# Kernel optimization log

Hardware: AMD Instinct MI355X
Metric: run time of the kernel (lower is better)

Reference implementation:

```python
import jax, jax.numpy as jnp
import numpy as np

N, E = 100000, 1600000
IN, H, OUT = 64, 64, 32
BN_EPS = 1e-5


def setup_inputs() -> dict:
    key = jax.random.key(0)
    ks = jax.random.split(key, 13)

    def w(k, shape, fan_in):
        return jax.random.uniform(k, shape, jnp.float32, -1.0, 1.0) / np.sqrt(fan_in)

    return {
        "x": jax.random.normal(ks[0], (N, IN), jnp.float32),
        "edge_index": jax.random.randint(ks[1], (2, E), 0, N, jnp.int32),
        "W1": w(ks[2], (IN, H), IN),
        "b1": jnp.zeros((H,), jnp.float32),
        "gamma": jnp.ones((H,), jnp.float32),
        "beta": jnp.zeros((H,), jnp.float32),
        "W2": w(ks[3], (H, H), H),
        "b2": jnp.zeros((H,), jnp.float32),
        "lin2_w": w(ks[4], (H, OUT), H),
        "lin2_b": w(ks[5], (OUT,), H),
        "lin3_w": w(ks[6], (OUT, H), OUT),
        "lin3_b": w(ks[7], (H,), OUT),
    }


def gcn_conv(x, src, dst, W, b):
    # PyG GCNConv: h = D^{-1/2} (A + I) D^{-1/2} (x W) + b
    n = x.shape[0]
    h = x @ W  # [N, H]
    loop = jnp.arange(n, dtype=src.dtype)
    s = jnp.concatenate([src, loop])  # add self-loops
    d = jnp.concatenate([dst, loop])
    deg = jax.ops.segment_sum(jnp.ones_like(s, x.dtype), d, num_segments=n)
    dinv = jnp.where(deg > 0, jax.lax.rsqrt(deg), 0.0)
    norm = dinv[s] * dinv[d]  # [E+N]
    msg = h[s] * norm[:, None]  # gather + scale
    out = jax.ops.segment_sum(msg, d, num_segments=n)  # scatter-add
    return out + b


def reference(x, edge_index, W1, b1, gamma, beta, W2, b2, lin2_w, lin2_b, lin3_w, lin3_b):
    src, dst = edge_index[0], edge_index[1]
    h = gcn_conv(x, src, dst, W1, b1)
    # BatchNorm1d in eval mode with default running stats (mean=0, var=1)
    h = gamma * (h * jax.lax.rsqrt(jnp.float32(1.0 + BN_EPS))) + beta
    h = jax.nn.relu(h)  # dropout is identity in eval
    h = gcn_conv(h, src, dst, W2, b2)
    logits = h @ lin2_w + lin2_b  # [N, OUT]
    p = jax.nn.softmax(logits, axis=-1)
    ent = -jnp.sum(p * jnp.log(p + 1e-9), axis=-1)  # [N]
    wts = 1.0 / (ent + 1e-10)
    wts = (wts - wts.min()) / (wts.max() - wts.min())
    wts = jax.nn.softmax(wts, axis=0)  # [N]
    graph = jnp.sum(logits * wts[:, None], axis=0, keepdims=True)  # [1, OUT]
    return graph @ lin3_w + lin3_b  # [1, H]
```

## Files before the change

kernel.cpp:

```cpp
#include <hip/hip_runtime.h>
#include <hip/hip_bf16.h>
#include <hip/hip_fp8.h>
#include <math.h>


#define F 64
#define OUTF 32
#define PB 128
#define LEDGE 5632
#define WG 512
#define BN_INV 0.9999950000374997f
#define ESC_X 32.0f
#define IESC_X 0.03125f
#define ESC_Z 64.0f
#define IESC_Z 0.015625f

typedef short bf16x8 __attribute__((ext_vector_type(8)));
typedef float f32x4 __attribute__((ext_vector_type(4)));

__device__ __forceinline__ unsigned fenc(float f) {
    unsigned u = __float_as_uint(f);
    return (u & 0x80000000u) ? ~u : (u | 0x80000000u);
}
__device__ __forceinline__ float fdec(unsigned e) {
    return (e & 0x80000000u) ? __uint_as_float(e & 0x7fffffffu) : __uint_as_float(~e);
}
__device__ __forceinline__ unsigned short f2bf(float f) {
    unsigned u = __float_as_uint(f);
    return (unsigned short)((u + 0x7fffu + ((u >> 16) & 1u)) >> 16);
}
__device__ __forceinline__ float bf2f(unsigned short h) {
    return __uint_as_float((unsigned)h << 16);
}

#if __has_builtin(__builtin_amdgcn_cvt_f32_fp8) && __has_builtin(__builtin_amdgcn_cvt_pk_fp8_f32)
__device__ __forceinline__ float4 fp8x4(unsigned v) {
    return make_float4(__builtin_amdgcn_cvt_f32_fp8((int)v, 0),
                       __builtin_amdgcn_cvt_f32_fp8((int)v, 1),
                       __builtin_amdgcn_cvt_f32_fp8((int)v, 2),
                       __builtin_amdgcn_cvt_f32_fp8((int)v, 3));
}
__device__ __forceinline__ unsigned fp8pk4(float a, float b, float c, float d) {
    int r = __builtin_amdgcn_cvt_pk_fp8_f32(a, b, 0, false);
    r = __builtin_amdgcn_cvt_pk_fp8_f32(c, d, r, true);
    return (unsigned)r;
}
__device__ __forceinline__ unsigned char fp8enc1(float a) {
    return (unsigned char)(__builtin_amdgcn_cvt_pk_fp8_f32(a, a, 0, false) & 0xff);
}
#else
__device__ __forceinline__ float fp8d1(unsigned char b) {
    __hip_fp8_e4m3 v; v.__x = (__hip_fp8_storage_t)b; return (float)v;
}
__device__ __forceinline__ float4 fp8x4(unsigned v) {
    return make_float4(fp8d1(v & 255u), fp8d1((v >> 8) & 255u), fp8d1((v >> 16) & 255u), fp8d1((v >> 24) & 255u));
}
__device__ __forceinline__ unsigned char fp8enc1(float a) {
    return (unsigned char)__hip_fp8_e4m3(a).__x;
}
__device__ __forceinline__ unsigned fp8pk4(float a, float b, float c, float d) {
    return (unsigned)fp8enc1(a) | ((unsigned)fp8enc1(b) << 8) | ((unsigned)fp8enc1(c) << 16) | ((unsigned)fp8enc1(d) << 24);
}
#endif


__global__ __launch_bounds__(256) void k_hist(const int* __restrict__ dst, int* __restrict__ hist,
                                              int E, int NBK,
                                              const float* __restrict__ W1, const float* __restrict__ b1,
                                              const float* __restrict__ gamma, const float* __restrict__ beta,
                                              const float* __restrict__ W2, const float* __restrict__ b2,
                                              const float* __restrict__ l2w, const float* __restrict__ l2b,
                                              unsigned short* __restrict__ w1f, unsigned short* __restrict__ w2f,
                                              float* __restrict__ bias1f, float* __restrict__ b2l2,
                                              float* __restrict__ red) {
    __shared__ int lh[512];
    int t = threadIdx.x, blk = blockIdx.x;
    if (blk >= PB) {
        int tt = (blk - PB) * 256 + t;
        int k = tt >> 5, cc = tt & 31;
        float o = 0.0f;
        for (int j = 0; j < F; j++) o += W2[k * F + j] * l2w[j * OUTF + cc];
        {
            int t2 = cc >> 4, s = k >> 5, kb = (k >> 3) & 3, jj = k & 7;
            int ln = kb * 16 + (cc & 15);
            w2f[(size_t)((t2 * 2 + s) * 64 + ln) * 8 + jj] = f2bf(o);
        }
        for (int e = tt; e < F * F; e += 2048) {
            int kk = e >> 6, c = e & 63;
            float wv = W1[kk * F + c] * gamma[c] * BN_INV;
            int t1i = c >> 4, s = kk >> 5, kb = (kk >> 3) & 3, jj = kk & 7;
            int ln = kb * 16 + (c & 15);
            w1f[(size_t)((t1i * 2 + s) * 64 + ln) * 8 + jj] = f2bf(wv);
        }
        if (tt < F) bias1f[tt] = fmaf(b1[tt], gamma[tt] * BN_INV, beta[tt]);
        if (tt < OUTF) {
            float b = l2b[tt];
            for (int j = 0; j < F; j++) b += b2[j] * l2w[j * OUTF + tt];
            b2l2[tt] = b;
        }
        if (tt == 33) ((unsigned*)red)[33] = 0xFFFFFFFFu;
        if (tt == 34) ((unsigned*)red)[34] = 0u;
        return;
    }
    for (int b = t; b < NBK; b += 256) lh[b] = 0;
    __syncthreads();
    int chunk = (E + PB - 1) / PB;
    int beg = blk * chunk, end = min(beg + chunk, E);
    for (int e = beg + t; e < end; e += 256) atomicAdd(&lh[dst[e] >> 8], 1);
    __syncthreads();
    for (int b = t; b < NBK; b += 256) hist[blk * NBK + b] = lh[b];
}

__global__ __launch_bounds__(PB) void k_hscan1(int* __restrict__ hist, int* __restrict__ btot, int NBK) {
    __shared__ int s[PB];
    int b = blockIdx.x, t = threadIdx.x;
    int v = hist[t * NBK + b];
    s[t] = v;
    __syncthreads();
    for (int off = 1; off < PB; off <<= 1) {
        int u = (t >= off) ? s[t - off] : 0;
        __syncthreads();
        s[t] += u;
        __syncthreads();
    }
    hist[t * NBK + b] = s[t] - v;
    if (t == PB - 1) btot[b] = s[t];
}

__global__ void k_hscan2(const int* __restrict__ btot, int* __restrict__ bbase, int NBK) {
    __shared__ int s[512];
    int t = threadIdx.x;
    int v = (t < NBK) ? btot[t] : 0;
    s[t] = v;
    __syncthreads();
    for (int off = 1; off < 512; off <<= 1) {
        int u = (t >= off) ? s[t - off] : 0;
        __syncthreads();
        s[t] += u;
        __syncthreads();
    }
    if (t < NBK) {
        bbase[t] = s[t] - v;
        if (t == NBK - 1) bbase[NBK] = s[t];
    }
}

__global__ __launch_bounds__(256) void k_place(const int* __restrict__ src, const int* __restrict__ dst,
                                               const int* __restrict__ hist, const int* __restrict__ bbase,
                                               unsigned* __restrict__ bucketArr, int E, int NBK) {
    __shared__ int cur[512];
    int t = threadIdx.x, blk = blockIdx.x;
    for (int b = t; b < NBK; b += 256) cur[b] = hist[blk * NBK + b] + bbase[b];
    __syncthreads();
    int chunk = (E + PB - 1) / PB;
    int beg = blk * chunk, end = min(beg + chunk, E);
    for (int e = beg + t; e < end; e += 256) {
        int d = dst[e], sidx = src[e];
        int p = atomicAdd(&cur[d >> 8], 1);
        bucketArr[p] = ((unsigned)sidx << 8) | (unsigned)(d & 255);
    }
}

__global__ __launch_bounds__(256) void k_binsort(const unsigned* __restrict__ bucketArr,
                                                 const int* __restrict__ bbase,
                                                 int* __restrict__ eidx, int4* __restrict__ meta,
                                                 const float4* __restrict__ x4, unsigned* __restrict__ xq, int N) {
    __shared__ unsigned ledge[LEDGE];
    __shared__ int lcnt[256], lofs[256], lcur[256], lscan[256];
    __shared__ float ldinv[256];
    int b = blockIdx.x, t = threadIdx.x;
    int gb = bbase[b];
    int count = min(bbase[b + 1] - gb, LEDGE);
    for (int j = t; j < count; j += 256) ledge[j] = bucketArr[gb + j];
    lcnt[t] = 0;
    __syncthreads();
    for (int j = t; j < count; j += 256) atomicAdd(&lcnt[ledge[j] & 255u], 1);
    __syncthreads();
    int deg = lcnt[t];
    lscan[t] = deg;
    __syncthreads();
    for (int off = 1; off < 256; off <<= 1) {
        int u = (t >= off) ? lscan[t - off] : 0;
        __syncthreads();
        lscan[t] += u;
        __syncthreads();
    }
    lofs[t] = lscan[t] - deg;
    lcur[t] = 0;
    int node = (b << 8) + t;
    float di = rsqrtf((float)deg + 1.0f);
    ldinv[t] = di;
    if (node < N) meta[node] = make_int4(gb + lofs[t], deg, __float_as_int(di), 0);
    __syncthreads();
    for (int j = t; j < count; j += 256) {
        unsigned v = ledge[j];
        int loc = (int)(v & 255u);
        int p = atomicAdd(&lcur[loc], 1);
        eidx[gb + lofs[loc] + p] = (int)(v >> 8);
    }
    for (int idx = t; idx < 256 * 16; idx += 256) {
        int nd = (b << 8) + (idx >> 4);
        if (nd < N) {
            float d2 = ldinv[idx >> 4] * ESC_X;
            float4 v = x4[(size_t)nd * 16 + (idx & 15)];
            xq[(size_t)nd * 16 + (idx & 15)] = fp8pk4(v.x * d2, v.y * d2, v.z * d2, v.w * d2);
        }
    }
}

__global__ __launch_bounds__(256, 4) void k_conv1agg(const uint2* __restrict__ xq2,
                                                     const int4* __restrict__ meta,
                                                     const int* __restrict__ eidx,
                                                     unsigned short* __restrict__ t1, int N, int Em1) {
    int tid = threadIdx.x, wave = tid >> 6, lane = tid & 63;
    int g = lane >> 3, gl = lane & 7, gbase = lane & 56;
    int i = (blockIdx.x * 4 + wave) * 8 + g;
    int iclamp = min(i, N - 1);
    int4 m = meta[iclamp];
    int beg = m.x;
    int dcnt = (i < N) ? m.y : 0;
    float dis = __int_as_float(m.z) * IESC_X;
    int ss0 = eidx[min(beg + gl, Em1)];
    int ss1 = eidx[min(beg + 8 + gl, Em1)];
    int ss2 = eidx[min(beg + 16 + gl, Em1)];
    int ss3 = eidx[min(beg + 24 + gl, Em1)];
    uint2 selfv = xq2[(size_t)iclamp * 8 + gl];
    uint2 vbuf[32];
#pragma unroll
    for (int k = 0; k < 32; k++) {
        int sreg = (k < 8) ? ss0 : (k < 16) ? ss1 : (k < 24) ? ss2 : ss3;
        int sv = __shfl(sreg, gbase + (k & 7), 64);
        sv = (k < dcnt) ? sv : iclamp;
        vbuf[k] = xq2[(size_t)sv * 8 + gl];
    }
    __builtin_amdgcn_sched_barrier(0);
    float4 aA0 = fp8x4(selfv.x), aB0 = fp8x4(selfv.y);
    float4 aA1 = make_float4(0.f, 0.f, 0.f, 0.f), aB1 = aA1;
#pragma unroll
    for (int k = 0; k < 32; k++) {
        if (k < dcnt) {
            float4 vA = fp8x4(vbuf[k].x), vB = fp8x4(vbuf[k].y);
            if (k & 1) {
                aA1.x += vA.x; aA1.y += vA.y; aA1.z += vA.z; aA1.w += vA.w;
                aB1.x += vB.x; aB1.y += vB.y; aB1.z += vB.z; aB1.w += vB.w;
            } else {
                aA0.x += vA.x; aA0.y += vA.y; aA0.z += vA.z; aA0.w += vA.w;
                aB0.x += vB.x; aB0.y += vB.y; aB0.z += vB.z; aB0.w += vB.w;
            }
        }
    }
    for (int base = 32; base < dcnt; base += 8) {
        int j = base + gl;
        int ss = eidx[min(beg + j, Em1)];
        int cnt = min(dcnt - base, 8);
#pragma unroll
        for (int k = 0; k < 8; k++) {
            if (k < cnt) {
                int sv = __shfl(ss, gbase + k, 64);
                uint2 v = xq2[(size_t)sv * 8 + gl];
                float4 vA = fp8x4(v.x), vB = fp8x4(v.y);
                aA0.x += vA.x; aA0.y += vA.y; aA0.z += vA.z; aA0.w += vA.w;
                aB0.x += vB.x; aB0.y += vB.y; aB0.z += vB.z; aB0.w += vB.w;
            }
        }
    }
    if (i < N) {
        float4 oA, oB;
        oA.x = (aA0.x + aA1.x) * dis; oA.y = (aA0.y + aA1.y) * dis;
        oA.z = (aA0.z + aA1.z) * dis; oA.w = (aA0.w + aA1.w) * dis;
        oB.x = (aB0.x + aB1.x) * dis; oB.y = (aB0.y + aB1.y) * dis;
        oB.z = (aB0.z + aB1.z) * dis; oB.w = (aB0.w + aB1.w) * dis;
        uint4 ob;
        ob.x = (unsigned)f2bf(oA.x) | ((unsigned)f2bf(oA.y) << 16);
        ob.y = (unsigned)f2bf(oA.z) | ((unsigned)f2bf(oA.w) << 16);
        ob.z = (unsigned)f2bf(oB.x) | ((unsigned)f2bf(oB.y) << 16);
        ob.w = (unsigned)f2bf(oB.z) | ((unsigned)f2bf(oB.w) << 16);
        *(uint4*)(t1 + (size_t)i * F + gl * 8) = ob;
    }
}

__global__ __launch_bounds__(256) void k_zm(const unsigned short* __restrict__ t1bf,
                                            const int4* __restrict__ meta,
                                            const unsigned short* __restrict__ w1f,
                                            const unsigned short* __restrict__ w2f,
                                            const float* __restrict__ bias1f,
                                            unsigned char* __restrict__ z2q, int N) {
    __shared__ __align__(16) unsigned short hlds[4][16][72];
    __shared__ float ldin[4][16];
    int tid = threadIdx.x, wave = tid >> 6, lane = tid & 63;
    int cl = lane & 15, kb = lane >> 4;
    int ntiles = (N + 15) >> 4;
    int tile = blockIdx.x * 4 + wave;
    if (tile >= ntiles) return;
    int row0 = tile << 4;

    int ra = min(row0 + cl, N - 1);
    const bf16x8* arow = (const bf16x8*)(t1bf + (size_t)ra * F);
    bf16x8 a0 = arow[kb];
    bf16x8 a1 = arow[4 + kb];
    if (lane < 16) ldin[wave][lane] = __int_as_float(meta[min(row0 + lane, N - 1)].z);

    const bf16x8* w1v = (const bf16x8*)w1f;
    const bf16x8* w2v = (const bf16x8*)w2f;
    bf16x8 w1frag[8];
#pragma unroll
    for (int q = 0; q < 8; q++) w1frag[q] = w1v[q * 64 + lane];
    bf16x8 w2frag[4];
#pragma unroll
    for (int q = 0; q < 4; q++) w2frag[q] = w2v[q * 64 + lane];
    float bias_t[4];
#pragma unroll
    for (int t = 0; t < 4; t++) bias_t[t] = bias1f[t * 16 + cl];

    f32x4 acc[4] = {};
#pragma unroll
    for (int t = 0; t < 4; t++) {
        acc[t] = __builtin_amdgcn_mfma_f32_16x16x32_bf16(a0, w1frag[t * 2 + 0], acc[t], 0, 0, 0);
        acc[t] = __builtin_amdgcn_mfma_f32_16x16x32_bf16(a1, w1frag[t * 2 + 1], acc[t], 0, 0, 0);
    }
    float di[4];
#pragma unroll
    for (int j = 0; j < 4; j++) di[j] = ldin[wave][kb * 4 + j];
#pragma unroll
    for (int t = 0; t < 4; t++)
#pragma unroll
        for (int j = 0; j < 4; j++) {
            float h = fmaxf(acc[t][j] + bias_t[t], 0.0f) * di[j];
            hlds[wave][kb * 4 + j][t * 16 + cl] = f2bf(h);
        }
    bf16x8 h0 = *(const bf16x8*)&hlds[wave][cl][kb * 8];
    bf16x8 h1 = *(const bf16x8*)&hlds[wave][cl][32 + kb * 8];
    f32x4 accz[2] = {};
#pragma unroll
    for (int t2 = 0; t2 < 2; t2++) {
        accz[t2] = __builtin_amdgcn_mfma_f32_16x16x32_bf16(h0, w2frag[t2 * 2 + 0], accz[t2], 0, 0, 0);
        accz[t2] = __builtin_amdgcn_mfma_f32_16x16x32_bf16(h1, w2frag[t2 * 2 + 1], accz[t2], 0, 0, 0);
    }
#pragma unroll
    for (int t2 = 0; t2 < 2; t2++)
#pragma unroll
        for (int j = 0; j < 4; j++) {
            int r = row0 + kb * 4 + j;
            if (r < N) z2q[(size_t)r * OUTF + t2 * 16 + cl] = fp8enc1(accz[t2][j] * ESC_Z);
        }
}

__global__ __launch_bounds__(256, 4) void k_conv2agg(const uint2* __restrict__ z2q2,
                                                     const int4* __restrict__ meta,
                                                     const int* __restrict__ eidx, const float* __restrict__ b2l2,
                                                     unsigned short* __restrict__ logits_bf, float* __restrict__ wraw,
                                                     unsigned* __restrict__ redmm, int N, int Em1) {
    __shared__ float smn[4], smx[4];
    int tid = threadIdx.x, wave = tid >> 6, lane = tid & 63;
    int g = lane >> 2, gl = lane & 3, gbase = lane & 60;
    float4 bvA = ((const float4*)b2l2)[gl * 2];
    float4 bvB = ((const float4*)b2l2)[gl * 2 + 1];
    int i = (blockIdx.x * 4 + wave) * 16 + g;
    int iclamp = min(i, N - 1);
    int4 m = meta[iclamp];
    int beg = m.x;
    int dcnt = (i < N) ? m.y : 0;
    float dis = __int_as_float(m.z) * IESC_Z;
    int ss0 = eidx[min(beg + gl, Em1)];
    int ss1 = eidx[min(beg + 4 + gl, Em1)];
    int ss2 = eidx[min(beg + 8 + gl, Em1)];
    int ss3 = eidx[min(beg + 12 + gl, Em1)];
    int ss4 = eidx[min(beg + 16 + gl, Em1)];
    int ss5 = eidx[min(beg + 20 + gl, Em1)];
    uint2 selfv = z2q2[(size_t)iclamp * 4 + gl];
    uint2 vbuf[24];
#pragma unroll
    for (int k = 0; k < 24; k++) {
        int sreg = (k < 4) ? ss0 : (k < 8) ? ss1 : (k < 12) ? ss2 : (k < 16) ? ss3 : (k < 20) ? ss4 : ss5;
        int sv = __shfl(sreg, gbase + (k & 3), 64);
        sv = (k < dcnt) ? sv : iclamp;
        vbuf[k] = z2q2[(size_t)sv * 4 + gl];
    }
    __builtin_amdgcn_sched_barrier(0);
    float4 aA0 = fp8x4(selfv.x), aB0 = fp8x4(selfv.y);
    if (i >= N) { aA0 = make_float4(0.f, 0.f, 0.f, 0.f); aB0 = aA0; }
    float4 aA1 = make_float4(0.f, 0.f, 0.f, 0.f), aB1 = aA1;
#pragma unroll
    for (int k = 0; k < 24; k++) {
        if (k < dcnt) {
            float4 vA = fp8x4(vbuf[k].x), vB = fp8x4(vbuf[k].y);
            if (k & 1) {
                aA1.x += vA.x; aA1.y += vA.y; aA1.z += vA.z; aA1.w += vA.w;
                aB1.x += vB.x; aB1.y += vB.y; aB1.z += vB.z; aB1.w += vB.w;
            } else {
                aA0.x += vA.x; aA0.y += vA.y; aA0.z += vA.z; aA0.w += vA.w;
                aB0.x += vB.x; aB0.y += vB.y; aB0.z += vB.z; aB0.w += vB.w;
            }
        }
    }
    for (int base = 24; base < dcnt; base += 4) {
        int j = base + gl;
        int ss = eidx[min(beg + j, Em1)];
        int cnt = min(dcnt - base, 4);
#pragma unroll
        for (int k = 0; k < 4; k++) {
            if (k < cnt) {
                int sv = __shfl(ss, gbase + k, 64);
                uint2 v = z2q2[(size_t)sv * 4 + gl];
                float4 vA = fp8x4(v.x), vB = fp8x4(v.y);
                aA0.x += vA.x; aA0.y += vA.y; aA0.z += vA.z; aA0.w += vA.w;
                aB0.x += vB.x; aB0.y += vB.y; aB0.z += vB.z; aB0.w += vB.w;
            }
        }
    }
    float4 lgA, lgB;
    lgA.x = fmaf(aA0.x + aA1.x, dis, bvA.x);
    lgA.y = fmaf(aA0.y + aA1.y, dis, bvA.y);
    lgA.z = fmaf(aA0.z + aA1.z, dis, bvA.z);
    lgA.w = fmaf(aA0.w + aA1.w, dis, bvA.w);
    lgB.x = fmaf(aB0.x + aB1.x, dis, bvB.x);
    lgB.y = fmaf(aB0.y + aB1.y, dis, bvB.y);
    lgB.z = fmaf(aB0.z + aB1.z, dis, bvB.z);
    lgB.w = fmaf(aB0.w + aB1.w, dis, bvB.w);
    if (i < N) {
        uint4 ob;
        ob.x = (unsigned)f2bf(lgA.x) | ((unsigned)f2bf(lgA.y) << 16);
        ob.y = (unsigned)f2bf(lgA.z) | ((unsigned)f2bf(lgA.w) << 16);
        ob.z = (unsigned)f2bf(lgB.x) | ((unsigned)f2bf(lgB.y) << 16);
        ob.w = (unsigned)f2bf(lgB.z) | ((unsigned)f2bf(lgB.w) << 16);
        *(uint4*)(logits_bf + (size_t)i * OUTF + gl * 8) = ob;
    }
    float m8 = fmaxf(fmaxf(fmaxf(lgA.x, lgA.y), fmaxf(lgA.z, lgA.w)),
                     fmaxf(fmaxf(lgB.x, lgB.y), fmaxf(lgB.z, lgB.w)));
    for (int off = 2; off > 0; off >>= 1) m8 = fmaxf(m8, __shfl_xor(m8, off, 4));
    float p0 = expf(lgA.x - m8), p1 = expf(lgA.y - m8), p2 = expf(lgA.z - m8), p3 = expf(lgA.w - m8);
    float p4 = expf(lgB.x - m8), p5 = expf(lgB.y - m8), p6 = expf(lgB.z - m8), p7 = expf(lgB.w - m8);
    float s8 = p0 + p1 + p2 + p3 + p4 + p5 + p6 + p7;
    for (int off = 2; off > 0; off >>= 1) s8 += __shfl_xor(s8, off, 4);
    float inv = 1.0f / s8;
    float t0 = p0 * inv, t1v = p1 * inv, t2v = p2 * inv, t3 = p3 * inv;
    float t4 = p4 * inv, t5 = p5 * inv, t6 = p6 * inv, t7 = p7 * inv;
    float e8 = t0 * logf(t0 + 1e-9f) + t1v * logf(t1v + 1e-9f) + t2v * logf(t2v + 1e-9f) + t3 * logf(t3 + 1e-9f) +
               t4 * logf(t4 + 1e-9f) + t5 * logf(t5 + 1e-9f) + t6 * logf(t6 + 1e-9f) + t7 * logf(t7 + 1e-9f);
    for (int off = 2; off > 0; off >>= 1) e8 += __shfl_xor(e8, off, 4);
    float w = 1.0f / (-e8 + 1e-10f);
    float mn = INFINITY, mx = -INFINITY;
    if (i < N) {
        if (gl == 0) wraw[i] = w;
        mn = w;
        mx = w;
    }
    for (int off = 32; off > 0; off >>= 1) {
        mn = fminf(mn, __shfl_xor(mn, off, 64));
        mx = fmaxf(mx, __shfl_xor(mx, off, 64));
    }
    if (lane == 0) { smn[wave] = mn; smx[wave] = mx; }
    __syncthreads();
    if (tid == 0) {
        float a = fminf(fminf(smn[0], smn[1]), fminf(smn[2], smn[3]));
        float b = fmaxf(fmaxf(smx[0], smx[1]), fmaxf(smx[2], smx[3]));
        atomicMin(&redmm[33], fenc(a));
        atomicMax(&redmm[34], fenc(b));
    }
}

__global__ __launch_bounds__(256) void k_weight(const unsigned short* __restrict__ logits_bf,
                                                const float* __restrict__ wraw,
                                                const float* __restrict__ red,
                                                float* __restrict__ part, int N) {
    const unsigned* mm = (const unsigned*)red;
    float mn = fdec(mm[33]), mx = fdec(mm[34]);
    float inv = 1.0f / (mx - mn);
    int c = threadIdx.x & 31;
    int g = threadIdx.x >> 5;
    float acc = 0.0f, es = 0.0f;
    for (int r = blockIdx.x * 8 + g; r < N; r += gridDim.x * 8) {
        float e = expf((wraw[r] - mn) * inv);
        acc += e * bf2f(logits_bf[(size_t)r * OUTF + c]);
        if (c == 0) es += e;
    }
    __shared__ float sa[8][OUTF];
    __shared__ float se[8];
    sa[g][c] = acc;
    if (c == 0) se[g] = es;
    __syncthreads();
    if (g == 0) {
        float t = sa[0][c];
#pragma unroll
        for (int i = 1; i < 8; i++) t += sa[i][c];
        part[blockIdx.x * 36 + c] = t;
        if (c == 0) {
            float u = 0.0f;
#pragma unroll
            for (int i = 0; i < 8; i++) u += se[i];
            part[blockIdx.x * 36 + 32] = u;
        }
    }
}

__global__ __launch_bounds__(256) void k_final(const float* __restrict__ part,
                                               const float* __restrict__ w3, const float* __restrict__ b3,
                                               float* __restrict__ out) {
    __shared__ float sa[8][OUTF];
    __shared__ float se[8];
    __shared__ float facc[OUTF + 1];
    int tid = threadIdx.x;
    int g = tid >> 5, c = tid & 31;
    float acc = 0.0f, es = 0.0f;
    for (int p = g; p < WG; p += 8) {
        acc += part[p * 36 + c];
        if (c == 0) es += part[p * 36 + 32];
    }
    sa[g][c] = acc;
    if (c == 0) se[g] = es;
    __syncthreads();
    if (tid < OUTF) {
        float t = 0.0f;
#pragma unroll
        for (int i = 0; i < 8; i++) t += sa[i][tid];
        facc[tid] = t;
    }
    if (tid == 32) {
        float u = 0.0f;
#pragma unroll
        for (int i = 0; i < 8; i++) u += se[i];
        facc[OUTF] = u;
    }
    __syncthreads();
    if (tid < F) {
        float s = facc[OUTF];
        float o = b3[tid];
#pragma unroll
        for (int cc = 0; cc < OUTF; cc++) o += (facc[cc] / s) * w3[cc * F + tid];
        out[tid] = o;
    }
}

extern "C" void kernel_launch(void* const* d_in, const int* in_sizes, int n_in,
                              void* d_out, int out_size, void* d_ws, size_t ws_size,
                              hipStream_t stream) {
    const float* x     = (const float*)d_in[0];
    const int*   ei    = (const int*)d_in[1];
    const float* W1    = (const float*)d_in[2];
    const float* b1    = (const float*)d_in[3];
    const float* gamma = (const float*)d_in[4];
    const float* beta  = (const float*)d_in[5];
    const float* W2    = (const float*)d_in[6];
    const float* b2    = (const float*)d_in[7];
    const float* l2w   = (const float*)d_in[8];
    const float* l2b   = (const float*)d_in[9];
    const float* l3w   = (const float*)d_in[10];
    const float* l3b   = (const float*)d_in[11];

    int N = in_sizes[0] / F;
    int E = in_sizes[1] / 2;
    const int* src = ei;
    const int* dst = ei + E;
    int NBK = (N + 255) >> 8;

    char* p = (char*)d_ws;
    int* hist = (int*)p;                p += (size_t)PB * NBK * 4;
    int* btot = (int*)p;                p += 512 * 4;
    int* bbase = (int*)p;               p += 516 * 4;
    unsigned* bucketArr = (unsigned*)p; p += (size_t)E * 4;
    int4* meta = (int4*)p;              p += (size_t)N * 16;
    int* eidx = (int*)p;                p += (size_t)E * 4;
    float* red = (float*)p;             p += 64 * 4;
    float* part = (float*)p;            p += (size_t)WG * 36 * 4;
    unsigned short* w1f = (unsigned short*)p;  p += F * F * 2;
    unsigned short* w2f = (unsigned short*)p;  p += F * OUTF * 2;
    float* bias1f = (float*)p;          p += F * 4;
    float* b2l2 = (float*)p;            p += OUTF * 4 + 32;
    unsigned* xq = (unsigned*)p;        p += (size_t)N * F;
    unsigned short* t1bf = (unsigned short*)p; p += (size_t)N * F * 2;
    float* wraw = (float*)p;            p += (size_t)N * 4;
    unsigned char* z2q = (unsigned char*)xq;
    unsigned short* logits_bf = (unsigned short*)t1bf;

    k_hist<<<PB + 8, 256, 0, stream>>>(dst, hist, E, NBK, W1, b1, gamma, beta, W2, b2, l2w, l2b,
                                       w1f, w2f, bias1f, b2l2, red);
    k_hscan1<<<NBK, PB, 0, stream>>>(hist, btot, NBK);
    k_hscan2<<<1, 512, 0, stream>>>(btot, bbase, NBK);
    k_place<<<PB, 256, 0, stream>>>(src, dst, hist, bbase, bucketArr, E, NBK);
    k_binsort<<<NBK, 256, 0, stream>>>(bucketArr, bbase, eidx, meta, (const float4*)x, xq, N);

    k_conv1agg<<<(N + 31) / 32, 256, 0, stream>>>((const uint2*)xq, meta, eidx, t1bf, N, E - 1);
    int nt = (N + 15) >> 4;
    k_zm<<<(nt + 3) / 4, 256, 0, stream>>>(t1bf, meta, w1f, w2f, bias1f, z2q, N);
    k_conv2agg<<<(N + 63) / 64, 256, 0, stream>>>((const uint2*)z2q, meta, eidx, b2l2, logits_bf, wraw, (unsigned*)red, N, E - 1);

    k_weight<<<WG, 256, 0, stream>>>(logits_bf, wraw, red, part, N);
    k_final<<<1, 256, 0, stream>>>(part, l3w, l3b, (float*)d_out);
}
```

Measured before the change: 263.2 us.

## Process two node groups per wave in conv2 aggregation and drop atomic min/max

k_conv2agg now has each wave handle 32 nodes instead of 16. It issues both groups' neighbor gathers before consuming either, aiming for more memory-level parallelism per wave, and launch bounds drop to 2 blocks per SM to make room for the extra registers. The global atomic min/max on encoded floats is replaced by per-block partial min/max that k_weight reduces itself, which removes the reset in k_hist. expf/logf become the fast __expf/__logf intrinsics, trading some accuracy for cheaper transcendentals.

```diff
diff --git a/kernel.cpp b/kernel.cpp
--- a/kernel.cpp
+++ b/kernel.cpp
@@ -18,13 +18,6 @@
 typedef short bf16x8 __attribute__((ext_vector_type(8)));
 typedef float f32x4 __attribute__((ext_vector_type(4)));
 
-__device__ __forceinline__ unsigned fenc(float f) {
-    unsigned u = __float_as_uint(f);
-    return (u & 0x80000000u) ? ~u : (u | 0x80000000u);
-}
-__device__ __forceinline__ float fdec(unsigned e) {
-    return (e & 0x80000000u) ? __uint_as_float(e & 0x7fffffffu) : __uint_as_float(~e);
-}
 __device__ __forceinline__ unsigned short f2bf(float f) {
     unsigned u = __float_as_uint(f);
     return (unsigned short)((u + 0x7fffu + ((u >> 16) & 1u)) >> 16);
@@ -62,7 +55,6 @@
     return (unsigned)fp8enc1(a) | ((unsigned)fp8enc1(b) << 8) | ((unsigned)fp8enc1(c) << 16) | ((unsigned)fp8enc1(d) << 24);
 }
 #endif
-
 
 __global__ __launch_bounds__(256) void k_hist(const int* __restrict__ dst, int* __restrict__ hist,
                                               int E, int NBK,
@@ -71,8 +63,7 @@
                                               const float* __restrict__ W2, const float* __restrict__ b2,
                                               const float* __restrict__ l2w, const float* __restrict__ l2b,
                                               unsigned short* __restrict__ w1f, unsigned short* __restrict__ w2f,
-                                              float* __restrict__ bias1f, float* __restrict__ b2l2,
-                                              float* __restrict__ red) {
+                                              float* __restrict__ bias1f, float* __restrict__ b2l2) {
     __shared__ int lh[512];
     int t = threadIdx.x, blk = blockIdx.x;
     if (blk >= PB) {
@@ -98,8 +89,6 @@
             for (int j = 0; j < F; j++) b += b2[j] * l2w[j * OUTF + tt];
             b2l2[tt] = b;
         }
-        if (tt == 33) ((unsigned*)red)[33] = 0xFFFFFFFFu;
-        if (tt == 34) ((unsigned*)red)[34] = 0u;
         return;
     }
     for (int b = t; b < NBK; b += 256) lh[b] = 0;
@@ -345,38 +334,13 @@
         }
 }
 
-__global__ __launch_bounds__(256, 4) void k_conv2agg(const uint2* __restrict__ z2q2,
-                                                     const int4* __restrict__ meta,
-                                                     const int* __restrict__ eidx, const float* __restrict__ b2l2,
-                                                     unsigned short* __restrict__ logits_bf, float* __restrict__ wraw,
-                                                     unsigned* __restrict__ redmm, int N, int Em1) {
-    __shared__ float smn[4], smx[4];
-    int tid = threadIdx.x, wave = tid >> 6, lane = tid & 63;
-    int g = lane >> 2, gl = lane & 3, gbase = lane & 60;
-    float4 bvA = ((const float4*)b2l2)[gl * 2];
-    float4 bvB = ((const float4*)b2l2)[gl * 2 + 1];
-    int i = (blockIdx.x * 4 + wave) * 16 + g;
-    int iclamp = min(i, N - 1);
-    int4 m = meta[iclamp];
-    int beg = m.x;
-    int dcnt = (i < N) ? m.y : 0;
-    float dis = __int_as_float(m.z) * IESC_Z;
-    int ss0 = eidx[min(beg + gl, Em1)];
-    int ss1 = eidx[min(beg + 4 + gl, Em1)];
-    int ss2 = eidx[min(beg + 8 + gl, Em1)];
-    int ss3 = eidx[min(beg + 12 + gl, Em1)];
-    int ss4 = eidx[min(beg + 16 + gl, Em1)];
-    int ss5 = eidx[min(beg + 20 + gl, Em1)];
-    uint2 selfv = z2q2[(size_t)iclamp * 4 + gl];
-    uint2 vbuf[24];
-#pragma unroll
-    for (int k = 0; k < 24; k++) {
-        int sreg = (k < 4) ? ss0 : (k < 8) ? ss1 : (k < 12) ? ss2 : (k < 16) ? ss3 : (k < 20) ? ss4 : ss5;
-        int sv = __shfl(sreg, gbase + (k & 3), 64);
-        sv = (k < dcnt) ? sv : iclamp;
-        vbuf[k] = z2q2[(size_t)sv * 4 + gl];
-    }
-    __builtin_amdgcn_sched_barrier(0);
+__device__ __forceinline__ void conv2_consume(const uint2 (&vbuf)[24], uint2 selfv, int dcnt,
+                                              int i, int beg, float dis, int gl, int gbase,
+                                              const uint2* __restrict__ z2q2, const int* __restrict__ eidx,
+                                              int Em1, float4 bvA, float4 bvB,
+                                              unsigned short* __restrict__ logits_bf,
+                                              float* __restrict__ wraw,
+                                              float& mnW, float& mxW, int N) {
     float4 aA0 = fp8x4(selfv.x), aB0 = fp8x4(selfv.y);
     if (i >= N) { aA0 = make_float4(0.f, 0.f, 0.f, 0.f); aB0 = aA0; }
     float4 aA1 = make_float4(0.f, 0.f, 0.f, 0.f), aB1 = aA1;
@@ -428,49 +392,116 @@
     float m8 = fmaxf(fmaxf(fmaxf(lgA.x, lgA.y), fmaxf(lgA.z, lgA.w)),
                      fmaxf(fmaxf(lgB.x, lgB.y), fmaxf(lgB.z, lgB.w)));
     for (int off = 2; off > 0; off >>= 1) m8 = fmaxf(m8, __shfl_xor(m8, off, 4));
-    float p0 = expf(lgA.x - m8), p1 = expf(lgA.y - m8), p2 = expf(lgA.z - m8), p3 = expf(lgA.w - m8);
-    float p4 = expf(lgB.x - m8), p5 = expf(lgB.y - m8), p6 = expf(lgB.z - m8), p7 = expf(lgB.w - m8);
+    float p0 = __expf(lgA.x - m8), p1 = __expf(lgA.y - m8), p2 = __expf(lgA.z - m8), p3 = __expf(lgA.w - m8);
+    float p4 = __expf(lgB.x - m8), p5 = __expf(lgB.y - m8), p6 = __expf(lgB.z - m8), p7 = __expf(lgB.w - m8);
     float s8 = p0 + p1 + p2 + p3 + p4 + p5 + p6 + p7;
     for (int off = 2; off > 0; off >>= 1) s8 += __shfl_xor(s8, off, 4);
     float inv = 1.0f / s8;
     float t0 = p0 * inv, t1v = p1 * inv, t2v = p2 * inv, t3 = p3 * inv;
     float t4 = p4 * inv, t5 = p5 * inv, t6 = p6 * inv, t7 = p7 * inv;
-    float e8 = t0 * logf(t0 + 1e-9f) + t1v * logf(t1v + 1e-9f) + t2v * logf(t2v + 1e-9f) + t3 * logf(t3 + 1e-9f) +
-               t4 * logf(t4 + 1e-9f) + t5 * logf(t5 + 1e-9f) + t6 * logf(t6 + 1e-9f) + t7 * logf(t7 + 1e-9f);
+    float e8 = t0 * __logf(t0 + 1e-9f) + t1v * __logf(t1v + 1e-9f) + t2v * __logf(t2v + 1e-9f) + t3 * __logf(t3 + 1e-9f) +
+               t4 * __logf(t4 + 1e-9f) + t5 * __logf(t5 + 1e-9f) + t6 * __logf(t6 + 1e-9f) + t7 * __logf(t7 + 1e-9f);
     for (int off = 2; off > 0; off >>= 1) e8 += __shfl_xor(e8, off, 4);
     float w = 1.0f / (-e8 + 1e-10f);
-    float mn = INFINITY, mx = -INFINITY;
     if (i < N) {
         if (gl == 0) wraw[i] = w;
-        mn = w;
-        mx = w;
+        mnW = fminf(mnW, w);
+        mxW = fmaxf(mxW, w);
+    }
+}
+
+__global__ __launch_bounds__(256, 2) void k_conv2agg(const uint2* __restrict__ z2q2,
+                                                     const int4* __restrict__ meta,
+                                                     const int* __restrict__ eidx, const float* __restrict__ b2l2,
+                                                     unsigned short* __restrict__ logits_bf, float* __restrict__ wraw,
+                                                     float* __restrict__ mnmx, int N, int Em1) {
+    __shared__ float smn[4], smx[4];
+    int tid = threadIdx.x, wave = tid >> 6, lane = tid & 63;
+    int g = lane >> 2, gl = lane & 3, gbase = lane & 60;
+    float4 bvA = ((const float4*)b2l2)[gl * 2];
+    float4 bvB = ((const float4*)b2l2)[gl * 2 + 1];
+    int wgid = blockIdx.x * 4 + wave;
+    int i0 = wgid * 32 + g;
+    int i1 = wgid * 32 + 16 + g;
+    int i0c = min(i0, N - 1), i1c = min(i1, N - 1);
+    int4 m0 = meta[i0c], m1 = meta[i1c];
+    int beg0 = m0.x, beg1 = m1.x;
+    int d0 = (i0 < N) ? m0.y : 0;
+    int d1 = (i1 < N) ? m1.y : 0;
+    float dis0 = __int_as_float(m0.z) * IESC_Z;
+    float dis1 = __int_as_float(m1.z) * IESC_Z;
+    int sA0 = eidx[min(beg0 + gl, Em1)];
+    int sA1 = eidx[min(beg0 + 4 + gl, Em1)];
+    int sA2 = eidx[min(beg0 + 8 + gl, Em1)];
+    int sA3 = eidx[min(beg0 + 12 + gl, Em1)];
+    int sA4 = eidx[min(beg0 + 16 + gl, Em1)];
+    int sA5 = eidx[min(beg0 + 20 + gl, Em1)];
+    int sB0 = eidx[min(beg1 + gl, Em1)];
+    int sB1 = eidx[min(beg1 + 4 + gl, Em1)];
+    int sB2 = eidx[min(beg1 + 8 + gl, Em1)];
+    int sB3 = eidx[min(beg1 + 12 + gl, Em1)];
+    int sB4 = eidx[min(beg1 + 16 + gl, Em1)];
+    int sB5 = eidx[min(beg1 + 20 + gl, Em1)];
+    uint2 self0 = z2q2[(size_t)i0c * 4 + gl];
+    uint2 self1 = z2q2[(size_t)i1c * 4 + gl];
+    uint2 vb0[24], vb1[24];
+#pragma unroll
+    for (int k = 0; k < 24; k++) {
+        int sreg = (k < 4) ? sA0 : (k < 8) ? sA1 : (k < 12) ? sA2 : (k < 16) ? sA3 : (k < 20) ? sA4 : sA5;
+        int sv = __shfl(sreg, gbase + (k & 3), 64);
+        sv = (k < d0) ? sv : i0c;
+        vb0[k] = z2q2[(size_t)sv * 4 + gl];
+    }
+#pragma unroll
+    for (int k = 0; k < 24; k++) {
+        int sreg = (k < 4) ? sB0 : (k < 8) ? sB1 : (k < 12) ? sB2 : (k < 16) ? sB3 : (k < 20) ? sB4 : sB5;
+        int sv = __shfl(sreg, gbase + (k & 3), 64);
+        sv = (k < d1) ? sv : i1c;
+        vb1[k] = z2q2[(size_t)sv * 4 + gl];
+    }
+    __builtin_amdgcn_sched_barrier(0);
+    float mnW = INFINITY, mxW = -INFINITY;
+    conv2_consume(vb0, self0, d0, i0, beg0, dis0, gl, gbase, z2q2, eidx, Em1,
+                  bvA, bvB, logits_bf, wraw, mnW, mxW, N);
+    conv2_consume(vb1, self1, d1, i1, beg1, dis1, gl, gbase, z2q2, eidx, Em1,
+                  bvA, bvB, logits_bf, wraw, mnW, mxW, N);
+    for (int off = 32; off > 0; off >>= 1) {
+        mnW = fminf(mnW, __shfl_xor(mnW, off, 64));
+        mxW = fmaxf(mxW, __shfl_xor(mxW, off, 64));
+    }
+    if (lane == 0) { smn[wave] = mnW; smx[wave] = mxW; }
+    __syncthreads();
+    if (tid == 0) {
+        mnmx[blockIdx.x * 2]     = fminf(fminf(smn[0], smn[1]), fminf(smn[2], smn[3]));
+        mnmx[blockIdx.x * 2 + 1] = fmaxf(fmaxf(smx[0], smx[1]), fmaxf(smx[2], smx[3]));
+    }
+}
+
+__global__ __launch_bounds__(256) void k_weight(const unsigned short* __restrict__ logits_bf,
+                                                const float* __restrict__ wraw,
+                                                const float* __restrict__ mnmx, int nmm,
+                                                float* __restrict__ part, int N) {
+    __shared__ float rmn[4], rmx[4];
+    float mn = INFINITY, mx = -INFINITY;
+    for (int j = threadIdx.x; j < nmm; j += 256) {
+        mn = fminf(mn, mnmx[j * 2]);
+        mx = fmaxf(mx, mnmx[j * 2 + 1]);
     }
     for (int off = 32; off > 0; off >>= 1) {
         mn = fminf(mn, __shfl_xor(mn, off, 64));
         mx = fmaxf(mx, __shfl_xor(mx, off, 64));
     }
-    if (lane == 0) { smn[wave] = mn; smx[wave] = mx; }
-    __syncthreads();
-    if (tid == 0) {
-        float a = fminf(fminf(smn[0], smn[1]), fminf(smn[2], smn[3]));
-        float b = fmaxf(fmaxf(smx[0], smx[1]), fmaxf(smx[2], smx[3]));
-        atomicMin(&redmm[33], fenc(a));
-        atomicMax(&redmm[34], fenc(b));
-    }
-}
-
-__global__ __launch_bounds__(256) void k_weight(const unsigned short* __restrict__ logits_bf,
-                                                const float* __restrict__ wraw,
-                                                const float* __restrict__ red,
-                                                float* __restrict__ part, int N) {
-    const unsigned* mm = (const unsigned*)red;
-    float mn = fdec(mm[33]), mx = fdec(mm[34]);
+    int wv = threadIdx.x >> 6;
+    if ((threadIdx.x & 63) == 0) { rmn[wv] = mn; rmx[wv] = mx; }
+    __syncthreads();
+    mn = fminf(fminf(rmn[0], rmn[1]), fminf(rmn[2], rmn[3]));
+    mx = fmaxf(fmaxf(rmx[0], rmx[1]), fmaxf(rmx[2], rmx[3]));
     float inv = 1.0f / (mx - mn);
     int c = threadIdx.x & 31;
     int g = threadIdx.x >> 5;
     float acc = 0.0f, es = 0.0f;
     for (int r = blockIdx.x * 8 + g; r < N; r += gridDim.x * 8) {
-        float e = expf((wraw[r] - mn) * inv);
+        float e = __expf((wraw[r] - mn) * inv);
         acc += e * bf2f(logits_bf[(size_t)r * OUTF + c]);
         if (c == 0) es += e;
     }
@@ -560,7 +591,7 @@
     unsigned* bucketArr = (unsigned*)p; p += (size_t)E * 4;
     int4* meta = (int4*)p;              p += (size_t)N * 16;
     int* eidx = (int*)p;                p += (size_t)E * 4;
-    float* red = (float*)p;             p += 64 * 4;
+    float* mnmx = (float*)p;            p += 2048 * 4;
     float* part = (float*)p;            p += (size_t)WG * 36 * 4;
     unsigned short* w1f = (unsigned short*)p;  p += F * F * 2;
     unsigned short* w2f = (unsigned short*)p;  p += F * OUTF * 2;
@@ -573,7 +604,7 @@
     unsigned short* logits_bf = (unsigned short*)t1bf;
 
     k_hist<<<PB + 8, 256, 0, stream>>>(dst, hist, E, NBK, W1, b1, gamma, beta, W2, b2, l2w, l2b,
-                                       w1f, w2f, bias1f, b2l2, red);
+                                       w1f, w2f, bias1f, b2l2);
     k_hscan1<<<NBK, PB, 0, stream>>>(hist, btot, NBK);
     k_hscan2<<<1, 512, 0, stream>>>(btot, bbase, NBK);
     k_place<<<PB, 256, 0, stream>>>(src, dst, hist, bbase, bucketArr, E, NBK);
@@ -582,8 +613,10 @@
     k_conv1agg<<<(N + 31) / 32, 256, 0, stream>>>((const uint2*)xq, meta, eidx, t1bf, N, E - 1);
     int nt = (N + 15) >> 4;
     k_zm<<<(nt + 3) / 4, 256, 0, stream>>>(t1bf, meta, w1f, w2f, bias1f, z2q, N);
-    k_conv2agg<<<(N + 63) / 64, 256, 0, stream>>>((const uint2*)z2q, meta, eidx, b2l2, logits_bf, wraw, (unsigned*)red, N, E - 1);
-
-    k_weight<<<WG, 256, 0, stream>>>(logits_bf, wraw, red, part, N);
+    int wg2 = (nt + 1) >> 1;
+    int nb2 = (wg2 + 3) >> 2;
+    k_conv2agg<<<nb2, 256, 0, stream>>>((const uint2*)z2q, meta, eidx, b2l2, logits_bf, wraw, mnmx, N, E - 1);
+
+    k_weight<<<WG, 256, 0, stream>>>(logits_bf, wraw, mnmx, nb2, part, N);
     k_final<<<1, 256, 0, stream>>>(part, l3w, l3b, (float*)d_out);
 }
```

After: 243.5 us. 1.08x faster.
